# Kernel tuning notes

Measured on AMD Instinct MI355X. Metric: run time of the kernel, lower is better.

The kernel has to match this reference:

```python
import jax, jax.numpy as jnp
import numpy as np

SEQ_LEN, INPUT_SIZE, HIDDEN_SIZE, OUTPUT_SIZE = 2048, 1024, 2048, 512


def _xavier(key, shape):
    fan_out, fan_in = shape
    limit = jnp.sqrt(6.0 / (fan_in + fan_out)).astype(jnp.float32)
    return jax.random.uniform(key, shape, jnp.float32, -limit, limit)


def setup_inputs() -> dict:
    key = jax.random.key(0)
    ks = jax.random.split(key, 6)
    H, I, O = HIDDEN_SIZE, INPUT_SIZE, OUTPUT_SIZE
    return {
        "X": jax.random.normal(ks[0], (SEQ_LEN, I, 1), jnp.float32),
        "W_f": _xavier(ks[1], (H, H + I)),
        "b_f": jnp.zeros((H, 1), jnp.float32),
        "W_i": _xavier(ks[2], (H, H + I)),
        "b_i": jnp.zeros((H, 1), jnp.float32),
        "W_c": _xavier(ks[3], (H, H + I)),
        "b_c": jnp.zeros((H, 1), jnp.float32),
        "W_o": _xavier(ks[4], (H, H + I)),
        "b_o": jnp.zeros((H, 1), jnp.float32),
        "W_y": jax.random.normal(ks[5], (O, H), jnp.float32) * 0.01,
        "b_y": jnp.zeros((O, 1), jnp.float32),
    }


def reference(X, W_f, b_f, W_i, b_i, W_c, b_c, W_o, b_o, W_y, b_y):
    # Dropout is identity in eval mode.
    H = W_f.shape[0]
    h0 = jnp.zeros((H, 1), X.dtype)
    c0 = jnp.zeros((H, 1), X.dtype)

    def step(carry, x_t):
        h, c = carry
        z = jnp.concatenate([h, x_t], axis=0)          # (H+I, 1)
        f = jax.nn.sigmoid(W_f @ z + b_f)
        i = jax.nn.sigmoid(W_i @ z + b_i)
        c_cand = jnp.tanh(W_c @ z + b_c)
        c = f * c + i * c_cand
        o = jax.nn.sigmoid(W_o @ z + b_o)
        h = o * jnp.tanh(c)
        y = W_y @ h + b_y                               # (O, 1)
        return (h, c), (y, h)

    _, (outputs, hidden_states) = jax.lax.scan(step, (h0, c0), X)
    return outputs, hidden_states
```

## Files before the change

### kernel.cpp

```cpp
#include <hip/hip_runtime.h>
#include <stdint.h>

#define SEQ  2048
#define HID  2048
#define INP  1024
#define OUTW 512
#define SENT 0x7F7F7F7Fu

__device__ __forceinline__ unsigned short f2bf(float x){
  unsigned int u = __float_as_uint(x);
  u += 0x7fffu + ((u >> 16) & 1u);
  return (unsigned short)(u >> 16);
}
__device__ __forceinline__ float bf_lo(unsigned int w){ return __uint_as_float(w << 16); }
__device__ __forceinline__ float bf_hi(unsigned int w){ return __uint_as_float(w & 0xffff0000u); }

__global__ __launch_bounds__(256)
void fill_hist(uint4* __restrict__ hist4){
  size_t i = (size_t)blockIdx.x*blockDim.x + threadIdx.x;
  hist4[i] = make_uint4(SENT,SENT,SENT,SENT);
}

__global__ __launch_bounds__(256)
void xproj_gemm(const float* __restrict__ Wf, const float* __restrict__ Wi,
                const float* __restrict__ Wc, const float* __restrict__ Wo,
                const float* __restrict__ bfv, const float* __restrict__ biv,
                const float* __restrict__ bcv, const float* __restrict__ bov,
                const float* __restrict__ X, unsigned short* __restrict__ xproj)
{
  __shared__ float As[16][68];
  __shared__ float Bs[16][68];
  const int t0 = blockIdx.x * 64;
  const int r0 = blockIdx.y * 64;
  const int gate = r0 >> 11;
  const int j0 = r0 & 2047;
  const float* Wg = gate==0?Wf:gate==1?Wi:gate==2?Wc:Wo;
  const float* bg = gate==0?bfv:gate==1?biv:gate==2?bcv:bov;
  const int tid = threadIdx.x;
  const int tx = tid & 15, ty = tid >> 4;
  const int lr = tid >> 2;
  const int lk = (tid & 3) * 4;
  float acc[4][4] = {};
  for (int k0 = 0; k0 < INP; k0 += 16){
    float4 av = *(const float4*)(Wg + (size_t)(j0+lr)*3072 + 2048 + k0 + lk);
    float4 bv = *(const float4*)(X  + (size_t)(t0+lr)*INP  + k0 + lk);
    __syncthreads();
    As[lk+0][lr]=av.x; As[lk+1][lr]=av.y; As[lk+2][lr]=av.z; As[lk+3][lr]=av.w;
    Bs[lk+0][lr]=bv.x; Bs[lk+1][lr]=bv.y; Bs[lk+2][lr]=bv.z; Bs[lk+3][lr]=bv.w;
    __syncthreads();
    #pragma unroll
    for (int kk=0;kk<16;kk++){
      float a[4], bb[4];
      #pragma unroll
      for (int i=0;i<4;i++) a[i]  = As[kk][ty*4+i];
      #pragma unroll
      for (int j=0;j<4;j++) bb[j] = Bs[kk][tx*4+j];
      #pragma unroll
      for (int i=0;i<4;i++)
        #pragma unroll
        for (int j=0;j<4;j++)
          acc[i][j] = fmaf(a[i], bb[j], acc[i][j]);
    }
  }
  #pragma unroll
  for (int i=0;i<4;i++){
    int j = j0 + ty*4 + i;
    float bias = bg[j];
    int bb = j >> 3, u = j & 7;
    #pragma unroll
    for (int jj=0;jj<4;jj++){
      int t = t0 + tx*4 + jj;
      size_t idx = (((size_t)bb*SEQ + t)*8 + u)*4 + gate;
      xproj[idx] = f2bf(acc[i][jj] + bias);
    }
  }
}

__global__ __launch_bounds__(512, 2)
void lstm_persistent(const float* __restrict__ Wf, const float* __restrict__ Wi,
                     const float* __restrict__ Wc, const float* __restrict__ Wo,
                     const unsigned short* __restrict__ xproj,
                     float* __restrict__ hist)
{
  const int b    = blockIdx.x;
  const int tid  = threadIdx.x;
  const int wv   = tid >> 6;
  const int lane = tid & 63;
  const int u    = b*8 + wv;

  __shared__ unsigned int h_lds[2][HID/2];

  const float* const Wm[4] = {Wf, Wi, Wc, Wo};
  float wreg[4][32];
  #pragma unroll
  for (int r=0;r<4;r++){
    const float* rowp = Wm[r] + (size_t)u*3072;
    #pragma unroll
    for (int kc=0;kc<4;kc++){
      float4 f0 = *(const float4*)(rowp + 8*lane + 512*kc);
      float4 f1 = *(const float4*)(rowp + 8*lane + 512*kc + 4);
      wreg[r][kc*8+0]=f0.x; wreg[r][kc*8+1]=f0.y; wreg[r][kc*8+2]=f0.z; wreg[r][kc*8+3]=f0.w;
      wreg[r][kc*8+4]=f1.x; wreg[r][kc*8+5]=f1.y; wreg[r][kc*8+6]=f1.z; wreg[r][kc*8+7]=f1.w;
    }
  }

  float c = 0.0f;
  const unsigned short* xpp = xproj + (size_t)b*SEQ*32 + wv*4 + lane;

  for (int t=0; t<SEQ; t++){
    float xp = (lane < 4) ? bf_lo((unsigned)xpp[(size_t)t*32]) : 0.0f;

    uint2 pk;
    if (t == 0){
      pk.x = 0u; pk.y = 0u;
    } else {
      const unsigned long long* hp =
        (const unsigned long long*)(hist + (size_t)(t-1)*HID) + 2*tid;
      unsigned long long qa = __hip_atomic_load(hp,   __ATOMIC_RELAXED, __HIP_MEMORY_SCOPE_AGENT);
      unsigned long long qb = __hip_atomic_load(hp+1, __ATOMIC_RELAXED, __HIP_MEMORY_SCOPE_AGENT);
      int gd = 0;
      for(;;){
        bool ba = ((unsigned)qa==SENT) | ((unsigned)(qa>>32)==SENT);
        bool bb = ((unsigned)qb==SENT) | ((unsigned)(qb>>32)==SENT);
        if (!(ba|bb) || gd >= (1<<17)) break;
        if (ba) qa = __hip_atomic_load(hp,   __ATOMIC_RELAXED, __HIP_MEMORY_SCOPE_AGENT);
        if (bb) qb = __hip_atomic_load(hp+1, __ATOMIC_RELAXED, __HIP_MEMORY_SCOPE_AGENT);
        gd++;
      }
      unsigned a0=(unsigned)qa, a1=(unsigned)(qa>>32), a2=(unsigned)qb, a3=(unsigned)(qb>>32);
      pk.x = (a1 & 0xffff0000u) | (a0 >> 16);
      pk.y = (a3 & 0xffff0000u) | (a2 >> 16);
    }
    const int p = t & 1;
    *(uint2*)&h_lds[p][2*tid] = pk;
    __syncthreads();

    float acc[4] = {0.f,0.f,0.f,0.f};
    #pragma unroll
    for (int kc=0;kc<4;kc++){
      uint4 hw = *(const uint4*)&h_lds[p][4*lane + 256*kc];
      float hf[8];
      hf[0]=bf_lo(hw.x); hf[1]=bf_hi(hw.x); hf[2]=bf_lo(hw.y); hf[3]=bf_hi(hw.y);
      hf[4]=bf_lo(hw.z); hf[5]=bf_hi(hw.z); hf[6]=bf_lo(hw.w); hf[7]=bf_hi(hw.w);
      #pragma unroll
      for (int r=0;r<4;r++)
        #pragma unroll
        for (int j=0;j<8;j++)
          acc[r] = fmaf(wreg[r][kc*8+j], hf[j], acc[r]);
    }

    const int b0 = lane & 1;
    const int b1 = lane & 2;
    float x01 = b0 ? acc[1] : acc[0];
    float y01 = b0 ? acc[0] : acc[1];
    x01 += __shfl_xor(y01, 1);
    float x23 = b0 ? acc[3] : acc[2];
    float y23 = b0 ? acc[2] : acc[3];
    x23 += __shfl_xor(y23, 1);
    float xk = b1 ? x23 : x01;
    float yk = b1 ? x01 : x23;
    xk += __shfl_xor(yk, 2);
    xk += __shfl_xor(xk, 4);
    xk += __shfl_xor(xk, 8);
    xk += __shfl_xor(xk, 16);
    xk += __shfl_xor(xk, 32);

    float pre = xk + __shfl(xp, lane & 3);
    const bool ist = ((lane & 3) == 2);
    float px = ist ? fminf(15.0f, fmaxf(-15.0f, pre)) : pre;
    float e  = __expf(ist ? -2.0f*px : -px);
    float d  = 1.0f/(1.0f + e);
    float gv = ist ? (1.0f - e)*d : d;

    float f  = __shfl(gv, 0);
    float ii = __shfl(gv, 1);
    float cg = __shfl(gv, 2);
    float o  = __shfl(gv, 3);

    c = fmaf(f, c, ii*cg);
    float cx = fminf(15.0f, fmaxf(-15.0f, c));
    float e2 = __expf(-2.0f*cx);
    float h  = o * (1.0f - e2)/(1.0f + e2);

    if (lane == 0)
      __hip_atomic_store(hist + (size_t)t*HID + u, h,
                         __ATOMIC_RELAXED, __HIP_MEMORY_SCOPE_AGENT);
  }
}

__global__ __launch_bounds__(256)
void ygemm(const float* __restrict__ hist, const float* __restrict__ Wy,
           const float* __restrict__ by, float* __restrict__ yout)
{
  __shared__ float As[16][68];
  __shared__ float Bs[16][68];
  const int o0 = blockIdx.x * 64;
  const int t0 = blockIdx.y * 64;
  const int tid = threadIdx.x;
  const int tx = tid & 15, ty = tid >> 4;
  const int lr = tid >> 2;
  const int lk = (tid & 3) * 4;
  float acc[4][4] = {};
  for (int k0 = 0; k0 < HID; k0 += 16){
    float4 av = *(const float4*)(hist + (size_t)(t0+lr)*HID + k0 + lk);
    float4 bv = *(const float4*)(Wy   + (size_t)(o0+lr)*HID + k0 + lk);
    __syncthreads();
    As[lk+0][lr]=av.x; As[lk+1][lr]=av.y; As[lk+2][lr]=av.z; As[lk+3][lr]=av.w;
    Bs[lk+0][lr]=bv.x; Bs[lk+1][lr]=bv.y; Bs[lk+2][lr]=bv.z; Bs[lk+3][lr]=bv.w;
    __syncthreads();
    #pragma unroll
    for (int kk=0;kk<16;kk++){
      float a[4], bb[4];
      #pragma unroll
      for (int i=0;i<4;i++) a[i]  = As[kk][ty*4+i];
      #pragma unroll
      for (int j=0;j<4;j++) bb[j] = Bs[kk][tx*4+j];
      #pragma unroll
      for (int i=0;i<4;i++)
        #pragma unroll
        for (int j=0;j<4;j++)
          acc[i][j] = fmaf(a[i], bb[j], acc[i][j]);
    }
  }
  #pragma unroll
  for (int i=0;i<4;i++){
    int t = t0 + ty*4 + i;
    #pragma unroll
    for (int jj=0;jj<4;jj++){
      int o = o0 + tx*4 + jj;
      yout[(size_t)t*OUTW + o] = acc[i][jj] + by[o];
    }
  }
}

extern "C" void kernel_launch(void* const* d_in, const int* in_sizes, int n_in,
                              void* d_out, int out_size, void* d_ws, size_t ws_size,
                              hipStream_t stream) {
  const float* X  = (const float*)d_in[0];
  const float* Wf = (const float*)d_in[1];
  const float* bf = (const float*)d_in[2];
  const float* Wi = (const float*)d_in[3];
  const float* bi = (const float*)d_in[4];
  const float* Wc = (const float*)d_in[5];
  const float* bc = (const float*)d_in[6];
  const float* Wo = (const float*)d_in[7];
  const float* bo = (const float*)d_in[8];
  const float* Wy = (const float*)d_in[9];
  const float* by = (const float*)d_in[10];

  float* yout = (float*)d_out;
  float* hist = (float*)d_out + (size_t)SEQ*OUTW;

  const size_t XPROJ_BYTES = (size_t)256*SEQ*32*sizeof(unsigned short);
  if (ws_size < XPROJ_BYTES) return;

  unsigned short* xproj = (unsigned short*)d_ws;

  fill_hist<<<(SEQ*(size_t)HID/4)/256, 256, 0, stream>>>((uint4*)hist);

  dim3 gA(32, 128);
  xproj_gemm<<<gA, 256, 0, stream>>>(Wf,Wi,Wc,Wo, bf,bi,bc,bo, X, xproj);
  lstm_persistent<<<256, 512, 0, stream>>>(Wf,Wi,Wc,Wo, xproj, hist);
  dim3 gY(8, 32);
  ygemm<<<gY, 256, 0, stream>>>(hist, Wy, by, yout);
}
```

Baseline: 4.783 ms.

## Exchange hidden state via bf16 sentinel buffer with single-wave polling per block

Adds a separate bf16 hidden-state exchange buffer in the workspace, prefilled with sentinels. In each block only wave 0 polls global memory for the previous step's hidden vector, detecting sentinel halves with a SWAR test. It then stages the vector in LDS and signals the other waves through a workgroup-scope flag. This halves the bytes polled per step and cuts redundant global polling by the other waves, at the cost of an extra LDS handoff and spin on a shared flag. The old path is kept as a fallback when the workspace is too small.

```diff
diff --git a/kernel.cpp b/kernel.cpp
--- a/kernel.cpp
+++ b/kernel.cpp
@@ -6,6 +6,7 @@
 #define INP  1024
 #define OUTW 512
 #define SENT 0x7F7F7F7Fu
+#define SENTH 0x7F7Fu
 
 __device__ __forceinline__ unsigned short f2bf(float x){
   unsigned int u = __float_as_uint(x);
@@ -14,11 +15,15 @@
 }
 __device__ __forceinline__ float bf_lo(unsigned int w){ return __uint_as_float(w << 16); }
 __device__ __forceinline__ float bf_hi(unsigned int w){ return __uint_as_float(w & 0xffff0000u); }
+__device__ __forceinline__ bool has_sent(unsigned long long x){
+  unsigned long long y = x ^ 0x7F7F7F7F7F7F7F7FULL;
+  return ((y - 0x0001000100010001ULL) & ~y & 0x8000800080008000ULL) != 0ULL;
+}
 
 __global__ __launch_bounds__(256)
-void fill_hist(uint4* __restrict__ hist4){
+void fill_sent(uint4* __restrict__ p){
   size_t i = (size_t)blockIdx.x*blockDim.x + threadIdx.x;
-  hist4[i] = make_uint4(SENT,SENT,SENT,SENT);
+  p[i] = make_uint4(SENT,SENT,SENT,SENT);
 }
 
 __global__ __launch_bounds__(256)
@@ -77,10 +82,161 @@
 }
 
 __global__ __launch_bounds__(512, 2)
-void lstm_persistent(const float* __restrict__ Wf, const float* __restrict__ Wi,
-                     const float* __restrict__ Wc, const float* __restrict__ Wo,
-                     const unsigned short* __restrict__ xproj,
-                     float* __restrict__ hist)
+void lstm_scan(const float* __restrict__ Wf, const float* __restrict__ Wi,
+               const float* __restrict__ Wc, const float* __restrict__ Wo,
+               const unsigned short* __restrict__ xproj,
+               unsigned short* __restrict__ hx,
+               float* __restrict__ hist)
+{
+  const int b    = blockIdx.x;
+  const int tid  = threadIdx.x;
+  const int wv   = tid >> 6;
+  const int lane = tid & 63;
+  const int u    = b*8 + wv;
+
+  __shared__ unsigned int h_lds[2][HID/2];
+  __shared__ int done;
+
+  if (tid == 0) done = -1;
+  __syncthreads();
+
+  const float* const Wm[4] = {Wf, Wi, Wc, Wo};
+  float wreg[4][32];
+  #pragma unroll
+  for (int r=0;r<4;r++){
+    const float* rowp = Wm[r] + (size_t)u*3072;
+    #pragma unroll
+    for (int kc=0;kc<4;kc++){
+      float4 f0 = *(const float4*)(rowp + 8*lane + 512*kc);
+      float4 f1 = *(const float4*)(rowp + 8*lane + 512*kc + 4);
+      wreg[r][kc*8+0]=f0.x; wreg[r][kc*8+1]=f0.y; wreg[r][kc*8+2]=f0.z; wreg[r][kc*8+3]=f0.w;
+      wreg[r][kc*8+4]=f1.x; wreg[r][kc*8+5]=f1.y; wreg[r][kc*8+6]=f1.z; wreg[r][kc*8+7]=f1.w;
+    }
+  }
+
+  float c = 0.0f;
+  const unsigned short* xpp = xproj + (size_t)b*SEQ*32 + wv*4 + lane;
+
+  for (int t=0; t<SEQ; t++){
+    float xp = (lane < 4) ? bf_lo((unsigned)xpp[(size_t)t*32]) : 0.0f;
+
+    uint4 hw0, hw1, hw2, hw3;
+    if (t == 0){
+      hw0 = hw1 = hw2 = hw3 = make_uint4(0u,0u,0u,0u);
+    } else if (wv == 0){
+      const char* hb = (const char*)(hx + (size_t)(t-1)*HID);
+      unsigned long long q[8];
+      #pragma unroll
+      for (int kc=0;kc<4;kc++){
+        const unsigned long long* p = (const unsigned long long*)(hb + 1024*kc + 16*lane);
+        q[2*kc]   = __hip_atomic_load(p,   __ATOMIC_RELAXED, __HIP_MEMORY_SCOPE_AGENT);
+        q[2*kc+1] = __hip_atomic_load(p+1, __ATOMIC_RELAXED, __HIP_MEMORY_SCOPE_AGENT);
+      }
+      int gd = 0;
+      for(;;){
+        bool bb[8]; bool any = false;
+        #pragma unroll
+        for (int i=0;i<8;i++){ bb[i] = has_sent(q[i]); any |= bb[i]; }
+        if (!any || gd >= (1<<17)) break;
+        #pragma unroll
+        for (int i=0;i<8;i++) if (bb[i]){
+          const unsigned long long* p =
+            (const unsigned long long*)(hb + 1024*(i>>1) + 16*lane + 8*(i&1));
+          q[i] = __hip_atomic_load(p, __ATOMIC_RELAXED, __HIP_MEMORY_SCOPE_AGENT);
+        }
+        gd++;
+      }
+      char* db = (char*)&h_lds[(t-1)&1][0];
+      uint4 v0, v1, v2, v3;
+      v0.x=(unsigned)q[0]; v0.y=(unsigned)(q[0]>>32); v0.z=(unsigned)q[1]; v0.w=(unsigned)(q[1]>>32);
+      v1.x=(unsigned)q[2]; v1.y=(unsigned)(q[2]>>32); v1.z=(unsigned)q[3]; v1.w=(unsigned)(q[3]>>32);
+      v2.x=(unsigned)q[4]; v2.y=(unsigned)(q[4]>>32); v2.z=(unsigned)q[5]; v2.w=(unsigned)(q[5]>>32);
+      v3.x=(unsigned)q[6]; v3.y=(unsigned)(q[6]>>32); v3.z=(unsigned)q[7]; v3.w=(unsigned)(q[7]>>32);
+      *(uint4*)(db +    0 + 16*lane) = v0;
+      *(uint4*)(db + 1024 + 16*lane) = v1;
+      *(uint4*)(db + 2048 + 16*lane) = v2;
+      *(uint4*)(db + 3072 + 16*lane) = v3;
+      hw0 = v0; hw1 = v1; hw2 = v2; hw3 = v3;
+      if (lane == 0)
+        __hip_atomic_store(&done, t-1, __ATOMIC_RELEASE, __HIP_MEMORY_SCOPE_WORKGROUP);
+    } else {
+      int g = 0;
+      while (__hip_atomic_load(&done, __ATOMIC_ACQUIRE, __HIP_MEMORY_SCOPE_WORKGROUP) < t-1
+             && g < (1<<20)) g++;
+      const char* rb = (const char*)&h_lds[(t-1)&1][0];
+      hw0 = *(const uint4*)(rb +    0 + 16*lane);
+      hw1 = *(const uint4*)(rb + 1024 + 16*lane);
+      hw2 = *(const uint4*)(rb + 2048 + 16*lane);
+      hw3 = *(const uint4*)(rb + 3072 + 16*lane);
+    }
+
+    float p0[4] = {0.f,0.f,0.f,0.f};
+    float p1[4] = {0.f,0.f,0.f,0.f};
+    const uint4 hws[4] = {hw0, hw1, hw2, hw3};
+    #pragma unroll
+    for (int kc=0;kc<4;kc++){
+      uint4 hw = hws[kc];
+      float hf[8];
+      hf[0]=bf_lo(hw.x); hf[1]=bf_hi(hw.x); hf[2]=bf_lo(hw.y); hf[3]=bf_hi(hw.y);
+      hf[4]=bf_lo(hw.z); hf[5]=bf_hi(hw.z); hf[6]=bf_lo(hw.w); hf[7]=bf_hi(hw.w);
+      #pragma unroll
+      for (int r=0;r<4;r++){
+        #pragma unroll
+        for (int j=0;j<4;j++) p0[r] = fmaf(wreg[r][kc*8+j],   hf[j],   p0[r]);
+        #pragma unroll
+        for (int j=0;j<4;j++) p1[r] = fmaf(wreg[r][kc*8+4+j], hf[4+j], p1[r]);
+      }
+    }
+    float acc[4];
+    #pragma unroll
+    for (int r=0;r<4;r++) acc[r] = p0[r] + p1[r];
+
+    const int b0 = lane & 1;
+    const int b1 = lane & 2;
+    float x01 = b0 ? acc[1] : acc[0];
+    float y01 = b0 ? acc[0] : acc[1];
+    x01 += __shfl_xor(y01, 1);
+    float x23 = b0 ? acc[3] : acc[2];
+    float y23 = b0 ? acc[2] : acc[3];
+    x23 += __shfl_xor(y23, 1);
+    float xk = b1 ? x23 : x01;
+    float yk = b1 ? x01 : x23;
+    xk += __shfl_xor(yk, 2);
+    xk += __shfl_xor(xk, 4);
+    xk += __shfl_xor(xk, 8);
+    xk += __shfl_xor(xk, 16);
+    xk += __shfl_xor(xk, 32);
+
+    float pre = xk + __shfl(xp, lane & 3);
+    const bool ist = ((lane & 3) == 2);
+    float px = ist ? fminf(15.0f, fmaxf(-15.0f, pre)) : pre;
+    float e  = __expf(ist ? -2.0f*px : -px);
+    float d  = 1.0f/(1.0f + e);
+    float gv = ist ? (1.0f - e)*d : d;
+
+    float f  = __shfl(gv, 0);
+    float ii = __shfl(gv, 1);
+    float cg = __shfl(gv, 2);
+    float o  = __shfl(gv, 3);
+
+    c = fmaf(f, c, ii*cg);
+    float cx = fminf(15.0f, fmaxf(-15.0f, c));
+    float e2 = __expf(-2.0f*cx);
+    float h  = o * (1.0f - e2)/(1.0f + e2);
+
+    if (lane == 0){
+      __hip_atomic_store(hx + (size_t)t*HID + u, f2bf(h),
+                         __ATOMIC_RELAXED, __HIP_MEMORY_SCOPE_AGENT);
+      hist[(size_t)t*HID + u] = h;
+    }
+  }
+}
+
+__global__ __launch_bounds__(512, 2)
+void lstm_persistent_fb(const float* __restrict__ Wf, const float* __restrict__ Wi,
+                        const float* __restrict__ Wc, const float* __restrict__ Wo,
+                        const unsigned short* __restrict__ xproj,
+                        float* __restrict__ hist)
 {
   const int b    = blockIdx.x;
   const int tid  = threadIdx.x;
@@ -252,15 +408,23 @@
   float* hist = (float*)d_out + (size_t)SEQ*OUTW;
 
   const size_t XPROJ_BYTES = (size_t)256*SEQ*32*sizeof(unsigned short);
+  const size_t HX_BYTES    = (size_t)SEQ*HID*sizeof(unsigned short);
   if (ws_size < XPROJ_BYTES) return;
 
   unsigned short* xproj = (unsigned short*)d_ws;
 
-  fill_hist<<<(SEQ*(size_t)HID/4)/256, 256, 0, stream>>>((uint4*)hist);
-
   dim3 gA(32, 128);
-  xproj_gemm<<<gA, 256, 0, stream>>>(Wf,Wi,Wc,Wo, bf,bi,bc,bo, X, xproj);
-  lstm_persistent<<<256, 512, 0, stream>>>(Wf,Wi,Wc,Wo, xproj, hist);
   dim3 gY(8, 32);
+
+  if (ws_size >= XPROJ_BYTES + HX_BYTES){
+    unsigned short* hx = (unsigned short*)((char*)d_ws + XPROJ_BYTES);
+    fill_sent<<<HX_BYTES/16/256, 256, 0, stream>>>((uint4*)hx);
+    xproj_gemm<<<gA, 256, 0, stream>>>(Wf,Wi,Wc,Wo, bf,bi,bc,bo, X, xproj);
+    lstm_scan<<<256, 512, 0, stream>>>(Wf,Wi,Wc,Wo, xproj, hx, hist);
+  } else {
+    fill_sent<<<((size_t)SEQ*HID*4)/16/256, 256, 0, stream>>>((uint4*)hist);
+    xproj_gemm<<<gA, 256, 0, stream>>>(Wf,Wi,Wc,Wo, bf,bi,bc,bo, X, xproj);
+    lstm_persistent_fb<<<256, 512, 0, stream>>>(Wf,Wi,Wc,Wo, xproj, hist);
+  }
   ygemm<<<gY, 256, 0, stream>>>(hist, Wy, by, yout);
 }
```

Result: slower. 12.30 ms (+157.2%).

## Fuse input projection and output GEMM into the persistent LSTM kernel

Applied to the files above, without the earlier changes.

Removes the separate input-projection GEMM and output GEMM kernels. Each timestep now computes the W·x contribution inside the recurrent loop: per-wave loads of X and the input-weight slices are issued before the h-polling wait so they can overlap it. After the last step, the same persistent blocks wait for the final hidden state and run the Y GEMM tile-wise. This removes launches and the bf16 xproj round-trip, but it adds global loads (16 float4 per lane per step) and extra FMAs on the serial critical path. It also leaves half the threads idle during the tail GEMM.

```diff
diff --git a/kernel.cpp b/kernel.cpp
--- a/kernel.cpp
+++ b/kernel.cpp
@@ -7,11 +7,6 @@
 #define OUTW 512
 #define SENT 0x7F7F7F7Fu
 
-__device__ __forceinline__ unsigned short f2bf(float x){
-  unsigned int u = __float_as_uint(x);
-  u += 0x7fffu + ((u >> 16) & 1u);
-  return (unsigned short)(u >> 16);
-}
 __device__ __forceinline__ float bf_lo(unsigned int w){ return __uint_as_float(w << 16); }
 __device__ __forceinline__ float bf_hi(unsigned int w){ return __uint_as_float(w & 0xffff0000u); }
 
@@ -21,66 +16,15 @@
   hist4[i] = make_uint4(SENT,SENT,SENT,SENT);
 }
 
-__global__ __launch_bounds__(256)
-void xproj_gemm(const float* __restrict__ Wf, const float* __restrict__ Wi,
+__global__ __launch_bounds__(512, 2)
+void lstm_fused(const float* __restrict__ Wf, const float* __restrict__ Wi,
                 const float* __restrict__ Wc, const float* __restrict__ Wo,
                 const float* __restrict__ bfv, const float* __restrict__ biv,
                 const float* __restrict__ bcv, const float* __restrict__ bov,
-                const float* __restrict__ X, unsigned short* __restrict__ xproj)
-{
-  __shared__ float As[16][68];
-  __shared__ float Bs[16][68];
-  const int t0 = blockIdx.x * 64;
-  const int r0 = blockIdx.y * 64;
-  const int gate = r0 >> 11;
-  const int j0 = r0 & 2047;
-  const float* Wg = gate==0?Wf:gate==1?Wi:gate==2?Wc:Wo;
-  const float* bg = gate==0?bfv:gate==1?biv:gate==2?bcv:bov;
-  const int tid = threadIdx.x;
-  const int tx = tid & 15, ty = tid >> 4;
-  const int lr = tid >> 2;
-  const int lk = (tid & 3) * 4;
-  float acc[4][4] = {};
-  for (int k0 = 0; k0 < INP; k0 += 16){
-    float4 av = *(const float4*)(Wg + (size_t)(j0+lr)*3072 + 2048 + k0 + lk);
-    float4 bv = *(const float4*)(X  + (size_t)(t0+lr)*INP  + k0 + lk);
-    __syncthreads();
-    As[lk+0][lr]=av.x; As[lk+1][lr]=av.y; As[lk+2][lr]=av.z; As[lk+3][lr]=av.w;
-    Bs[lk+0][lr]=bv.x; Bs[lk+1][lr]=bv.y; Bs[lk+2][lr]=bv.z; Bs[lk+3][lr]=bv.w;
-    __syncthreads();
-    #pragma unroll
-    for (int kk=0;kk<16;kk++){
-      float a[4], bb[4];
-      #pragma unroll
-      for (int i=0;i<4;i++) a[i]  = As[kk][ty*4+i];
-      #pragma unroll
-      for (int j=0;j<4;j++) bb[j] = Bs[kk][tx*4+j];
-      #pragma unroll
-      for (int i=0;i<4;i++)
-        #pragma unroll
-        for (int j=0;j<4;j++)
-          acc[i][j] = fmaf(a[i], bb[j], acc[i][j]);
-    }
-  }
-  #pragma unroll
-  for (int i=0;i<4;i++){
-    int j = j0 + ty*4 + i;
-    float bias = bg[j];
-    int bb = j >> 3, u = j & 7;
-    #pragma unroll
-    for (int jj=0;jj<4;jj++){
-      int t = t0 + tx*4 + jj;
-      size_t idx = (((size_t)bb*SEQ + t)*8 + u)*4 + gate;
-      xproj[idx] = f2bf(acc[i][jj] + bias);
-    }
-  }
-}
-
-__global__ __launch_bounds__(512, 2)
-void lstm_persistent(const float* __restrict__ Wf, const float* __restrict__ Wi,
-                     const float* __restrict__ Wc, const float* __restrict__ Wo,
-                     const unsigned short* __restrict__ xproj,
-                     float* __restrict__ hist)
+                const float* __restrict__ X,  const float* __restrict__ Wy,
+                const float* __restrict__ byv,
+                float* __restrict__ hist,
+                float* __restrict__ yout)
 {
   const int b    = blockIdx.x;
   const int tid  = threadIdx.x;
@@ -89,6 +33,8 @@
   const int u    = b*8 + wv;
 
   __shared__ unsigned int h_lds[2][HID/2];
+  __shared__ float As[16][68];
+  __shared__ float Bs[16][68];
 
   const float* const Wm[4] = {Wf, Wi, Wc, Wo};
   float wreg[4][32];
@@ -104,11 +50,33 @@
     }
   }
 
+  float bias_sel;
+  {
+    float b0=bfv[u], b1=biv[u], b2=bcv[u], b3=bov[u];
+    int gg = lane & 3;
+    bias_sel = (gg==0) ? b0 : (gg==1) ? b1 : (gg==2) ? b2 : b3;
+  }
+
+  const float* wxb0 = Wf + (size_t)u*3072 + 2048 + 16*lane;
+  const float* wxb1 = Wi + (size_t)u*3072 + 2048 + 16*lane;
+  const float* wxb2 = Wc + (size_t)u*3072 + 2048 + 16*lane;
+  const float* wxb3 = Wo + (size_t)u*3072 + 2048 + 16*lane;
+  const float* xb   = X + 16*lane;
+
   float c = 0.0f;
-  const unsigned short* xpp = xproj + (size_t)b*SEQ*32 + wv*4 + lane;
 
   for (int t=0; t<SEQ; t++){
-    float xp = (lane < 4) ? bf_lo((unsigned)xpp[(size_t)t*32]) : 0.0f;
+    const float* xr = xb + (size_t)t*INP;
+    float4 xv0 = *(const float4*)(xr+0),  xv1 = *(const float4*)(xr+4);
+    float4 xv2 = *(const float4*)(xr+8),  xv3 = *(const float4*)(xr+12);
+    float4 w0a = *(const float4*)(wxb0+0), w0b = *(const float4*)(wxb0+4),
+           w0c = *(const float4*)(wxb0+8), w0d = *(const float4*)(wxb0+12);
+    float4 w1a = *(const float4*)(wxb1+0), w1b = *(const float4*)(wxb1+4),
+           w1c = *(const float4*)(wxb1+8), w1d = *(const float4*)(wxb1+12);
+    float4 w2a = *(const float4*)(wxb2+0), w2b = *(const float4*)(wxb2+4),
+           w2c = *(const float4*)(wxb2+8), w2d = *(const float4*)(wxb2+12);
+    float4 w3a = *(const float4*)(wxb3+0), w3b = *(const float4*)(wxb3+4),
+           w3c = *(const float4*)(wxb3+8), w3d = *(const float4*)(wxb3+12);
 
     uint2 pk;
     if (t == 0){
@@ -135,7 +103,27 @@
     *(uint2*)&h_lds[p][2*tid] = pk;
     __syncthreads();
 
-    float acc[4] = {0.f,0.f,0.f,0.f};
+    float xpart[4];
+    {
+      xpart[0] = w0a.x*xv0.x + w0a.y*xv0.y + w0a.z*xv0.z + w0a.w*xv0.w
+               + w0b.x*xv1.x + w0b.y*xv1.y + w0b.z*xv1.z + w0b.w*xv1.w
+               + w0c.x*xv2.x + w0c.y*xv2.y + w0c.z*xv2.z + w0c.w*xv2.w
+               + w0d.x*xv3.x + w0d.y*xv3.y + w0d.z*xv3.z + w0d.w*xv3.w;
+      xpart[1] = w1a.x*xv0.x + w1a.y*xv0.y + w1a.z*xv0.z + w1a.w*xv0.w
+               + w1b.x*xv1.x + w1b.y*xv1.y + w1b.z*xv1.z + w1b.w*xv1.w
+               + w1c.x*xv2.x + w1c.y*xv2.y + w1c.z*xv2.z + w1c.w*xv2.w
+               + w1d.x*xv3.x + w1d.y*xv3.y + w1d.z*xv3.z + w1d.w*xv3.w;
+      xpart[2] = w2a.x*xv0.x + w2a.y*xv0.y + w2a.z*xv0.z + w2a.w*xv0.w
+               + w2b.x*xv1.x + w2b.y*xv1.y + w2b.z*xv1.z + w2b.w*xv1.w
+               + w2c.x*xv2.x + w2c.y*xv2.y + w2c.z*xv2.z + w2c.w*xv2.w
+               + w2d.x*xv3.x + w2d.y*xv3.y + w2d.z*xv3.z + w2d.w*xv3.w;
+      xpart[3] = w3a.x*xv0.x + w3a.y*xv0.y + w3a.z*xv0.z + w3a.w*xv0.w
+               + w3b.x*xv1.x + w3b.y*xv1.y + w3b.z*xv1.z + w3b.w*xv1.w
+               + w3c.x*xv2.x + w3c.y*xv2.y + w3c.z*xv2.z + w3c.w*xv2.w
+               + w3d.x*xv3.x + w3d.y*xv3.y + w3d.z*xv3.z + w3d.w*xv3.w;
+    }
+
+    float acc[4] = {xpart[0], xpart[1], xpart[2], xpart[3]};
     #pragma unroll
     for (int kc=0;kc<4;kc++){
       uint4 hw = *(const uint4*)&h_lds[p][4*lane + 256*kc];
@@ -165,7 +153,7 @@
     xk += __shfl_xor(xk, 16);
     xk += __shfl_xor(xk, 32);
 
-    float pre = xk + __shfl(xp, lane & 3);
+    float pre = xk + bias_sel;
     const bool ist = ((lane & 3) == 2);
     float px = ist ? fminf(15.0f, fmaxf(-15.0f, pre)) : pre;
     float e  = __expf(ist ? -2.0f*px : -px);
@@ -186,49 +174,64 @@
       __hip_atomic_store(hist + (size_t)t*HID + u, h,
                          __ATOMIC_RELAXED, __HIP_MEMORY_SCOPE_AGENT);
   }
-}
-
-__global__ __launch_bounds__(256)
-void ygemm(const float* __restrict__ hist, const float* __restrict__ Wy,
-           const float* __restrict__ by, float* __restrict__ yout)
-{
-  __shared__ float As[16][68];
-  __shared__ float Bs[16][68];
-  const int o0 = blockIdx.x * 64;
-  const int t0 = blockIdx.y * 64;
-  const int tid = threadIdx.x;
-  const int tx = tid & 15, ty = tid >> 4;
-  const int lr = tid >> 2;
+
+  {
+    const unsigned long long* hp =
+      (const unsigned long long*)(hist + (size_t)(SEQ-1)*HID) + 2*tid;
+    unsigned long long qa = __hip_atomic_load(hp,   __ATOMIC_RELAXED, __HIP_MEMORY_SCOPE_AGENT);
+    unsigned long long qb = __hip_atomic_load(hp+1, __ATOMIC_RELAXED, __HIP_MEMORY_SCOPE_AGENT);
+    int gd = 0;
+    for(;;){
+      bool ba = ((unsigned)qa==SENT) | ((unsigned)(qa>>32)==SENT);
+      bool bb = ((unsigned)qb==SENT) | ((unsigned)(qb>>32)==SENT);
+      if (!(ba|bb) || gd >= (1<<17)) break;
+      if (ba) qa = __hip_atomic_load(hp,   __ATOMIC_RELAXED, __HIP_MEMORY_SCOPE_AGENT);
+      if (bb) qb = __hip_atomic_load(hp+1, __ATOMIC_RELAXED, __HIP_MEMORY_SCOPE_AGENT);
+      gd++;
+    }
+  }
+  __syncthreads();
+
+  const int t0 = (b >> 3) * 64;
+  const int o0 = (b & 7) * 64;
+  const int tx = tid & 15, ty = (tid >> 4) & 15;
+  const int lr = (tid & 255) >> 2;
   const int lk = (tid & 3) * 4;
-  float acc[4][4] = {};
+  float yacc[4][4] = {};
   for (int k0 = 0; k0 < HID; k0 += 16){
-    float4 av = *(const float4*)(hist + (size_t)(t0+lr)*HID + k0 + lk);
-    float4 bv = *(const float4*)(Wy   + (size_t)(o0+lr)*HID + k0 + lk);
+    if (tid < 256){
+      float4 av = *(const float4*)(hist + (size_t)(t0+lr)*HID + k0 + lk);
+      float4 bv = *(const float4*)(Wy   + (size_t)(o0+lr)*HID + k0 + lk);
+      As[lk+0][lr]=av.x; As[lk+1][lr]=av.y; As[lk+2][lr]=av.z; As[lk+3][lr]=av.w;
+      Bs[lk+0][lr]=bv.x; Bs[lk+1][lr]=bv.y; Bs[lk+2][lr]=bv.z; Bs[lk+3][lr]=bv.w;
+    }
     __syncthreads();
-    As[lk+0][lr]=av.x; As[lk+1][lr]=av.y; As[lk+2][lr]=av.z; As[lk+3][lr]=av.w;
-    Bs[lk+0][lr]=bv.x; Bs[lk+1][lr]=bv.y; Bs[lk+2][lr]=bv.z; Bs[lk+3][lr]=bv.w;
+    if (tid < 256){
+      #pragma unroll
+      for (int kk=0;kk<16;kk++){
+        float a[4], bb2[4];
+        #pragma unroll
+        for (int i=0;i<4;i++) a[i]   = As[kk][ty*4+i];
+        #pragma unroll
+        for (int j=0;j<4;j++) bb2[j] = Bs[kk][tx*4+j];
+        #pragma unroll
+        for (int i=0;i<4;i++)
+          #pragma unroll
+          for (int j=0;j<4;j++)
+            yacc[i][j] = fmaf(a[i], bb2[j], yacc[i][j]);
+      }
+    }
     __syncthreads();
+  }
+  if (tid < 256){
     #pragma unroll
-    for (int kk=0;kk<16;kk++){
-      float a[4], bb[4];
+    for (int i=0;i<4;i++){
+      int t = t0 + ty*4 + i;
       #pragma unroll
-      for (int i=0;i<4;i++) a[i]  = As[kk][ty*4+i];
-      #pragma unroll
-      for (int j=0;j<4;j++) bb[j] = Bs[kk][tx*4+j];
-      #pragma unroll
-      for (int i=0;i<4;i++)
-        #pragma unroll
-        for (int j=0;j<4;j++)
-          acc[i][j] = fmaf(a[i], bb[j], acc[i][j]);
-    }
-  }
-  #pragma unroll
-  for (int i=0;i<4;i++){
-    int t = t0 + ty*4 + i;
-    #pragma unroll
-    for (int jj=0;jj<4;jj++){
-      int o = o0 + tx*4 + jj;
-      yout[(size_t)t*OUTW + o] = acc[i][jj] + by[o];
+      for (int jj=0;jj<4;jj++){
+        int o = o0 + tx*4 + jj;
+        yout[(size_t)t*OUTW + o] = yacc[i][jj] + byv[o];
+      }
     }
   }
 }
@@ -251,16 +254,8 @@
   float* yout = (float*)d_out;
   float* hist = (float*)d_out + (size_t)SEQ*OUTW;
 
-  const size_t XPROJ_BYTES = (size_t)256*SEQ*32*sizeof(unsigned short);
-  if (ws_size < XPROJ_BYTES) return;
-
-  unsigned short* xproj = (unsigned short*)d_ws;
-
   fill_hist<<<(SEQ*(size_t)HID/4)/256, 256, 0, stream>>>((uint4*)hist);
 
-  dim3 gA(32, 128);
-  xproj_gemm<<<gA, 256, 0, stream>>>(Wf,Wi,Wc,Wo, bf,bi,bc,bo, X, xproj);
-  lstm_persistent<<<256, 512, 0, stream>>>(Wf,Wi,Wc,Wo, xproj, hist);
-  dim3 gY(8, 32);
-  ygemm<<<gY, 256, 0, stream>>>(hist, Wy, by, yout);
+  lstm_fused<<<256, 512, 0, stream>>>(Wf,Wi,Wc,Wo, bf,bi,bc,bo,
+                                      X, Wy, by, hist, yout);
 }
```

Result: slower. 11.17 ms (+133.7%).
